# Kernel tuning notes

Hardware: AMD Instinct MI355X
Metric: run time of the kernel (lower is better)

The kernel has to match this reference:

```python
import jax, jax.numpy as jnp
import numpy as np

N = 100000
E = 1600000
G = 128


def _degrees(src, dst, n):
    ones = jnp.ones(src.shape[0], dtype=jnp.float32)
    deg_out = jax.ops.segment_sum(ones, src, num_segments=n)
    deg_in = jax.ops.segment_sum(ones, dst, num_segments=n)
    return jnp.maximum(deg_out, 1.0), jnp.maximum(deg_in, 1.0)


def gcn_conv(x, W, b, src, dst, norm_out, norm_in):
    # DGL GraphConv, norm='both': scale src by d_out^-1/2, sum over edges,
    # scale dst by d_in^-1/2, then linear. Weight applied first (out<=in) --
    # mathematically identical, cheaper gather.
    h = (x * norm_out[:, None]) @ W          # [N, out]
    m = h[src]                               # [E, out] gather
    agg = jax.ops.segment_sum(m, dst, num_segments=N)  # [N, out] scatter-add
    return agg * norm_in[:, None] + b


def setup_inputs() -> dict:
    key = jax.random.key(0)
    ks = jax.random.split(key, 8)
    x = jax.random.normal(ks[0], (N, 128), dtype=jnp.float32)
    W1 = jax.random.normal(ks[1], (128, 64), dtype=jnp.float32) * (1.0 / np.sqrt(128))
    b1 = jnp.zeros((64,), dtype=jnp.float32)
    W2 = jax.random.normal(ks[2], (64, 16), dtype=jnp.float32) * (1.0 / np.sqrt(64))
    b2 = jnp.zeros((16,), dtype=jnp.float32)
    src = jax.random.randint(ks[3], (E,), 0, N, dtype=jnp.int32)
    dst = jax.random.randint(ks[4], (E,), 0, N, dtype=jnp.int32)
    graph_ids = jnp.sort(jax.random.randint(ks[5], (N,), 0, G, dtype=jnp.int32))
    return {"x": x, "W1": W1, "b1": b1, "W2": W2, "b2": b2,
            "src": src, "dst": dst, "graph_ids": graph_ids}


def reference(x, W1, b1, W2, b2, src, dst, graph_ids):
    deg_out, deg_in = _degrees(src, dst, N)
    norm_out = jax.lax.rsqrt(deg_out)
    norm_in = jax.lax.rsqrt(deg_in)
    h = gcn_conv(x, W1, b1, src, dst, norm_out, norm_in)
    h = jax.nn.relu(h)
    # dropout(p=0.2) is identity in eval mode
    h = gcn_conv(h, W2, b2, src, dst, norm_out, norm_in)
    # dgl.mean_nodes: per-graph mean pooling
    sums = jax.ops.segment_sum(h, graph_ids, num_segments=G)      # [G, 16]
    counts = jax.ops.segment_sum(jnp.ones((N,), jnp.float32), graph_ids, num_segments=G)
    return sums / jnp.maximum(counts, 1.0)[:, None]
```

## Files before the change

### kernel.cpp

```cpp
#include <hip/hip_runtime.h>
#include <hip/hip_fp16.h>

#define N_NODES 100000
#define N_EDGES 1600000
#define N_GRAPHS 128
#define SB 391
#define CAP 4608
#define NBLK 512
#define NE4 (N_EDGES / 4)
#define CH4 782
#define LDX 136

typedef unsigned long long u64;
typedef unsigned int u32;
typedef unsigned char u8;
typedef _Float16 f16;
typedef f16 half8 __attribute__((ext_vector_type(8)));
typedef f16 half4v __attribute__((ext_vector_type(4)));
typedef f16 half2v __attribute__((ext_vector_type(2)));
typedef float floatx4 __attribute__((ext_vector_type(4)));

__global__ void k_init(int* __restrict__ cur_d, int* __restrict__ cur_s) {
  int t = blockIdx.x * blockDim.x + threadIdx.x;
  if (t < SB) { cur_d[t] = t * CAP; cur_s[t] = t * CAP; }
}

__global__ __launch_bounds__(256) void k_fuse(const int4* __restrict__ src4,
                                              const int4* __restrict__ dst4,
                                              int* __restrict__ cur_d,
                                              int* __restrict__ cur_s,
                                              u32* __restrict__ ed,
                                              u8* __restrict__ ssk8) {
  __shared__ int hd[SB], hs[SB], ld[SB], ls[SB];
  const int t = threadIdx.x, b = blockIdx.x;
  for (int j = t; j < SB; j += 256) { hd[j] = 0; hs[j] = 0; }
  __syncthreads();
  const int start = b * CH4, end = min(start + CH4, NE4);
  for (int i = start + t; i < end; i += 256) {
    int4 d = dst4[i]; int4 s = src4[i];
    atomicAdd(&hd[d.x >> 8], 1); atomicAdd(&hd[d.y >> 8], 1);
    atomicAdd(&hd[d.z >> 8], 1); atomicAdd(&hd[d.w >> 8], 1);
    atomicAdd(&hs[s.x >> 8], 1); atomicAdd(&hs[s.y >> 8], 1);
    atomicAdd(&hs[s.z >> 8], 1); atomicAdd(&hs[s.w >> 8], 1);
  }
  __syncthreads();
  for (int j = t; j < SB; j += 256) {
    ld[j] = atomicAdd(&cur_d[j], hd[j]);
    ls[j] = atomicAdd(&cur_s[j], hs[j]);
  }
  __syncthreads();
  for (int i = start + t; i < end; i += 256) {
    int4 d4 = dst4[i]; int4 s4 = src4[i];
    {
      int d = d4.x, s = s4.x;
      int pd = atomicAdd(&ld[d >> 8], 1);
      ed[pd] = ((u32)(d & 255) << 24) | (u32)s;
      int ps = atomicAdd(&ls[s >> 8], 1);
      ssk8[ps] = (u8)(s & 255);
    }
    {
      int d = d4.y, s = s4.y;
      int pd = atomicAdd(&ld[d >> 8], 1);
      ed[pd] = ((u32)(d & 255) << 24) | (u32)s;
      int ps = atomicAdd(&ls[s >> 8], 1);
      ssk8[ps] = (u8)(s & 255);
    }
    {
      int d = d4.z, s = s4.z;
      int pd = atomicAdd(&ld[d >> 8], 1);
      ed[pd] = ((u32)(d & 255) << 24) | (u32)s;
      int ps = atomicAdd(&ls[s >> 8], 1);
      ssk8[ps] = (u8)(s & 255);
    }
    {
      int d = d4.w, s = s4.w;
      int pd = atomicAdd(&ld[d >> 8], 1);
      ed[pd] = ((u32)(d & 255) << 24) | (u32)s;
      int ps = atomicAdd(&ls[s >> 8], 1);
      ssk8[ps] = (u8)(s & 255);
    }
  }
}

__global__ __launch_bounds__(256) void k_bucket_csr(const u32* __restrict__ ed,
                                                    const u8* __restrict__ ssk8,
                                                    const int* __restrict__ cur_d,
                                                    const int* __restrict__ cur_s,
                                                    int* __restrict__ row_ptr,
                                                    int* __restrict__ deg,
                                                    float* __restrict__ norm_in,
                                                    float* __restrict__ norm_out,
                                                    int* __restrict__ edge_src) {
  __shared__ int hist[256], scanbuf[256], cursor[256], hist2[256];
  const int b = blockIdx.x, t = threadIdx.x;
  const int base = b << 8;
  const int lo = b * CAP;
  const int hiD = cur_d[b];
  const int hiS = cur_s[b];
  hist[t] = 0; hist2[t] = 0;
  __syncthreads();
  for (int i = lo + t; i < hiS; i += 256) atomicAdd(&hist2[ssk8[i]], 1);
  for (int i = lo + t; i < hiD; i += 256) atomicAdd(&hist[ed[i] >> 24], 1);
  __syncthreads();
  int node = base + t;
  if (node < N_NODES)
    norm_out[node] = rsqrtf(fmaxf((float)hist2[t], 1.0f));
  int v = hist[t];
  scanbuf[t] = v;
  __syncthreads();
  for (int off = 1; off < 256; off <<= 1) {
    int a = (t >= off) ? scanbuf[t - off] : 0;
    __syncthreads(); scanbuf[t] += a; __syncthreads();
  }
  int excl = scanbuf[t] - v;
  if (node < N_NODES) {
    row_ptr[node] = lo + excl;
    deg[node] = v;
    norm_in[node] = rsqrtf(fmaxf((float)v, 1.0f));
  }
  cursor[t] = excl;
  __syncthreads();
  for (int i = lo + t; i < hiD; i += 256) {
    u32 e = ed[i];
    int p = atomicAdd(&cursor[e >> 24], 1);
    edge_src[lo + p] = (int)(e & 0x00FFFFFFu);
  }
}

__global__ __launch_bounds__(256) void k_gemm1(const float* __restrict__ x,
                                               const float* __restrict__ W1,
                                               const float* __restrict__ norm_out,
                                               __half* __restrict__ h1h) {
  __shared__ __align__(16) f16 Xs[64 * LDX];
  __shared__ __align__(16) f16 Ws[64 * LDX];
  const int t = threadIdx.x;
  const int row0 = blockIdx.x * 64;

  const float4* W4 = (const float4*)W1;
  for (int i = t; i < 2048; i += 256) {
    int k = i >> 4, n4 = (i & 15) * 4;
    float4 v = W4[i];
    Ws[(n4 + 0) * LDX + k] = (f16)v.x;
    Ws[(n4 + 1) * LDX + k] = (f16)v.y;
    Ws[(n4 + 2) * LDX + k] = (f16)v.z;
    Ws[(n4 + 3) * LDX + k] = (f16)v.w;
  }
  const float4* x4 = (const float4*)x;
  #pragma unroll
  for (int i = 0; i < 8; ++i) {
    int idx = t + 256 * i;
    int r = idx >> 5, c4 = idx & 31;
    int row = row0 + r;
    float4 v = make_float4(0.f, 0.f, 0.f, 0.f);
    if (row < N_NODES) {
      float s = norm_out[row];
      v = x4[(size_t)row * 32 + c4];
      v.x *= s; v.y *= s; v.z *= s; v.w *= s;
    }
    half4v h = { (f16)v.x, (f16)v.y, (f16)v.z, (f16)v.w };
    *(half4v*)&Xs[r * LDX + c4 * 4] = h;
  }
  __syncthreads();

  const int w = t >> 6, l = t & 63;
  const int m = l & 15, quad = l >> 4;
  floatx4 c0 = {0.f,0.f,0.f,0.f}, c1 = {0.f,0.f,0.f,0.f};
  floatx4 c2 = {0.f,0.f,0.f,0.f}, c3 = {0.f,0.f,0.f,0.f};
  const f16* xrow = &Xs[(w * 16 + m) * LDX + quad * 8];
  const f16* wrow = &Ws[m * LDX + quad * 8];
  #pragma unroll
  for (int kb = 0; kb < 4; ++kb) {
    half8 a  = *(const half8*)(xrow + kb * 32);
    half8 b0 = *(const half8*)(wrow + kb * 32);
    half8 b1 = *(const half8*)(wrow + 16 * LDX + kb * 32);
    half8 b2 = *(const half8*)(wrow + 32 * LDX + kb * 32);
    half8 b3 = *(const half8*)(wrow + 48 * LDX + kb * 32);
    c0 = __builtin_amdgcn_mfma_f32_16x16x32_f16(a, b0, c0, 0, 0, 0);
    c1 = __builtin_amdgcn_mfma_f32_16x16x32_f16(a, b1, c1, 0, 0, 0);
    c2 = __builtin_amdgcn_mfma_f32_16x16x32_f16(a, b2, c2, 0, 0, 0);
    c3 = __builtin_amdgcn_mfma_f32_16x16x32_f16(a, b3, c3, 0, 0, 0);
  }
  #pragma unroll
  for (int r = 0; r < 4; ++r) {
    int row = row0 + w * 16 + quad * 4 + r;
    if (row < N_NODES + 1) {
      __half* dst = h1h + (size_t)row * 64 + m;
      dst[0]  = __float2half(c0[r]);
      dst[16] = __float2half(c1[r]);
      dst[32] = __float2half(c2[r]);
      dst[48] = __float2half(c3[r]);
    }
  }
}

__global__ __launch_bounds__(256) void k_gather_l1(const int* __restrict__ row_ptr,
                                                   const int* __restrict__ deg,
                                                   const int* __restrict__ edge_src,
                                                   const __half* __restrict__ h1h,
                                                   const float* __restrict__ norm_in,
                                                   const float* __restrict__ norm_out,
                                                   const float* __restrict__ b1,
                                                   const float* __restrict__ W2,
                                                   __half* __restrict__ h2h) {
  __shared__ __align__(16) f16 Rs[16 * 72];
  __shared__ __align__(16) f16 Ws2[16 * 72];
  const int t = threadIdx.x;
  for (int i = t; i < 1024; i += 256) {
    int k = i >> 4, n = i & 15;
    Ws2[n * 72 + k] = (f16)W2[i];
  }
  if (blockIdx.x == 0 && t < 16) h2h[(size_t)N_NODES * 16 + t] = __float2half(0.f);

  const int w = t >> 6;
  const int l = t & 63;
  const int hf = l >> 5;
  const u32 c = (u32)(l & 31);

  const u32* __restrict__ h1u = (const u32*)h1h;
  const float2 bb = ((const float2*)b1)[c];
  const int base = blockIdx.x * 16;

  #pragma unroll 1
  for (int i4 = 0; i4 < 4; ++i4) {
    const int n = base + w * 4 + i4;
    const int lo = row_ptr[n], hi = lo + deg[n];

    float2 a0 = {0.f,0.f}, a1 = {0.f,0.f}, a2 = {0.f,0.f}, a3 = {0.f,0.f};
    float2 a4 = {0.f,0.f}, a5 = {0.f,0.f}, a6 = {0.f,0.f}, a7 = {0.f,0.f};
    for (int i = lo; i < hi; i += 16) {
      int idx = i + (l & 15);
      int sv = (idx < hi) ? edge_src[idx] : (int)N_NODES;
      int s0 = __shfl(sv,  0 + hf, 64);
      int s1 = __shfl(sv,  2 + hf, 64);
      int s2 = __shfl(sv,  4 + hf, 64);
      int s3 = __shfl(sv,  6 + hf, 64);
      int s4 = __shfl(sv,  8 + hf, 64);
      int s5 = __shfl(sv, 10 + hf, 64);
      int s6 = __shfl(sv, 12 + hf, 64);
      int s7 = __shfl(sv, 14 + hf, 64);
      u32 v0 = h1u[(u32)s0 * 32u + c];
      u32 v1 = h1u[(u32)s1 * 32u + c];
      u32 v2 = h1u[(u32)s2 * 32u + c];
      u32 v3 = h1u[(u32)s3 * 32u + c];
      u32 v4 = h1u[(u32)s4 * 32u + c];
      u32 v5 = h1u[(u32)s5 * 32u + c];
      u32 v6 = h1u[(u32)s6 * 32u + c];
      u32 v7 = h1u[(u32)s7 * 32u + c];
      float2 f;
      f = __half22float2(*(__half2*)&v0); a0.x += f.x; a0.y += f.y;
      f = __half22float2(*(__half2*)&v1); a1.x += f.x; a1.y += f.y;
      f = __half22float2(*(__half2*)&v2); a2.x += f.x; a2.y += f.y;
      f = __half22float2(*(__half2*)&v3); a3.x += f.x; a3.y += f.y;
      f = __half22float2(*(__half2*)&v4); a4.x += f.x; a4.y += f.y;
      f = __half22float2(*(__half2*)&v5); a5.x += f.x; a5.y += f.y;
      f = __half22float2(*(__half2*)&v6); a6.x += f.x; a6.y += f.y;
      f = __half22float2(*(__half2*)&v7); a7.x += f.x; a7.y += f.y;
    }
    float accx = ((a0.x + a1.x) + (a2.x + a3.x)) + ((a4.x + a5.x) + (a6.x + a7.x));
    float accy = ((a0.y + a1.y) + (a2.y + a3.y)) + ((a4.y + a5.y) + (a6.y + a7.y));
    accx += __shfl_xor(accx, 32, 64);
    accy += __shfl_xor(accy, 32, 64);

    const float ni = norm_in[n];
    float h1x = fmaxf(accx * ni + bb.x, 0.0f);
    float h1y = fmaxf(accy * ni + bb.y, 0.0f);
    if (l < 32) {
      half2v hv = { (f16)h1x, (f16)h1y };
      *(half2v*)&Rs[(w * 4 + i4) * 72 + 2 * (int)c] = hv;
    }
  }
  __syncthreads();

  if (w == 0) {
    const int m = l & 15, q = l >> 4;
    const f16* ra = &Rs[m * 72 + q * 8];
    const f16* rb = &Ws2[m * 72 + q * 8];
    half8 a0 = *(const half8*)ra;
    half8 a1 = *(const half8*)(ra + 32);
    half8 b0 = *(const half8*)rb;
    half8 b1v = *(const half8*)(rb + 32);
    floatx4 cc = {0.f,0.f,0.f,0.f};
    cc = __builtin_amdgcn_mfma_f32_16x16x32_f16(a0, b0, cc, 0, 0, 0);
    cc = __builtin_amdgcn_mfma_f32_16x16x32_f16(a1, b1v, cc, 0, 0, 0);
    #pragma unroll
    for (int r = 0; r < 4; ++r) {
      int row = base + q * 4 + r;
      h2h[(size_t)row * 16 + m] = __float2half(cc[r] * norm_out[row]);
    }
  }
}

__global__ __launch_bounds__(256) void k_gather_l2(const int* __restrict__ row_ptr,
                                                   const int* __restrict__ deg,
                                                   const int* __restrict__ edge_src,
                                                   const __half* __restrict__ h2h,
                                                   const float* __restrict__ norm_in,
                                                   float* __restrict__ agg2) {
  const int t = threadIdx.x;
  const int w = t >> 6;
  const int l = t & 63;
  const int n = blockIdx.x * 4 + w;
  const int f2 = l & 7;
  const int p = l >> 3;

  const u32* __restrict__ h2u = (const u32*)h2h;
  const int lo = row_ptr[n], hi = lo + deg[n];

  float ax = 0.f, ay = 0.f, bx = 0.f, by = 0.f;
  for (int base = lo; base < hi; base += 16) {
    int i1 = base + p, i2 = base + p + 8;
    int s0 = (i1 < hi) ? edge_src[i1] : (int)N_NODES;
    int s1 = (i2 < hi) ? edge_src[i2] : (int)N_NODES;
    u32 v0 = h2u[(u32)s0 * 8u + (u32)f2];
    u32 v1 = h2u[(u32)s1 * 8u + (u32)f2];
    float2 g0 = __half22float2(*(__half2*)&v0);
    float2 g1 = __half22float2(*(__half2*)&v1);
    ax += g0.x; ay += g0.y;
    bx += g1.x; by += g1.y;
  }
  float sx = ax + bx, sy = ay + by;
  sx += __shfl_xor(sx, 8, 64);  sy += __shfl_xor(sy, 8, 64);
  sx += __shfl_xor(sx, 16, 64); sy += __shfl_xor(sy, 16, 64);
  sx += __shfl_xor(sx, 32, 64); sy += __shfl_xor(sy, 32, 64);
  if (l < 8) {
    float ni = norm_in[n];
    ((float2*)agg2)[(size_t)n * 8 + f2] = make_float2(sx * ni, sy * ni);
  }
}

__global__ __launch_bounds__(256) void k_pool(const float* __restrict__ agg2,
                                              const float* __restrict__ b2,
                                              const int* __restrict__ gid,
                                              float* __restrict__ out) {
  const int g = blockIdx.x;
  __shared__ int s_lo, s_hi;
  if (threadIdx.x == 0) {
    int a = 0, b = N_NODES;
    while (a < b) { int m = (a + b) >> 1; if (gid[m] < g) a = m + 1; else b = m; }
    s_lo = a;
    b = N_NODES;
    while (a < b) { int m = (a + b) >> 1; if (gid[m] < g + 1) a = m + 1; else b = m; }
    s_hi = a;
  }
  __syncthreads();
  const int lo = s_lo, hi = s_hi, cnt = hi - lo;
  const int j = threadIdx.x & 15;
  const int r = threadIdx.x >> 4;
  float acc = 0.f;
  for (int n = lo + r; n < hi; n += 16)
    acc += agg2[(size_t)n * 16 + j];

  __shared__ float red[256];
  red[threadIdx.x] = acc;
  __syncthreads();
  #pragma unroll
  for (int s = 8; s > 0; s >>= 1) {
    if (r < s) red[threadIdx.x] += red[threadIdx.x + s * 16];
    __syncthreads();
  }
  if (r == 0)
    out[g * 16 + j] = (cnt > 0) ? (red[j] / (float)cnt + b2[j]) : 0.0f;
}

extern "C" void kernel_launch(void* const* d_in, const int* in_sizes, int n_in,
                              void* d_out, int out_size, void* d_ws, size_t ws_size,
                              hipStream_t stream) {
  const float* x   = (const float*)d_in[0];
  const float* W1  = (const float*)d_in[1];
  const float* b1  = (const float*)d_in[2];
  const float* W2  = (const float*)d_in[3];
  const float* b2  = (const float*)d_in[4];
  const int*   src = (const int*)d_in[5];
  const int*   dst = (const int*)d_in[6];
  const int*   gid = (const int*)d_in[7];
  float* out = (float*)d_out;

  int* wsi = (int*)d_ws;
  float* wsf = (float*)d_ws;

  float* norm_out = wsf + 0;
  float* norm_in  = wsf + 100000;
  int*   row_ptr  = wsi + 200000;
  int*   deg      = wsi + 300000;
  int*   cur_d    = wsi + 400000;
  int*   cur_s    = wsi + 400400;
  int*   edge_src = wsi + 400800;
  const size_t S  = 2202528;
  u8*    ssk8     = (u8*)(wsi + S);
  u32*   ed       = (u32*)(wsi + S + 450432);
  __half* h1h     = (__half*)(wsi + S);
  __half* h2h     = (__half*)(wsi + S + 3200032);
  float*  agg2    = (float*)(wsi + S);

  const int4* src4 = (const int4*)src;
  const int4* dst4 = (const int4*)dst;

  k_init      <<<2, 256, 0, stream>>>(cur_d, cur_s);
  k_fuse      <<<NBLK, 256, 0, stream>>>(src4, dst4, cur_d, cur_s, ed, ssk8);
  k_bucket_csr<<<SB, 256, 0, stream>>>(ed, ssk8, cur_d, cur_s, row_ptr, deg,
                                       norm_in, norm_out, edge_src);
  k_gemm1     <<<(N_NODES + 64) / 64, 256, 0, stream>>>(x, W1, norm_out, h1h);
  k_gather_l1 <<<N_NODES / 16, 256, 0, stream>>>(row_ptr, deg, edge_src, h1h,
                                                 norm_in, norm_out, b1, W2, h2h);
  k_gather_l2 <<<N_NODES / 4, 256, 0, stream>>>(row_ptr, deg, edge_src, h2h,
                                                norm_in, agg2);
  k_pool      <<<N_GRAPHS, 256, 0, stream>>>(agg2, b2, gid, out);
}
```

Before: 266.5 us.

## Aggregate layer-1 neighbor features with MFMA segment-sum over contiguous CSR edge ranges

Rewrites the layer-1 gather so that each wave handles 16 consecutive destination nodes as one contiguous edge range. Neighbor rows are loaded as 16-byte vectors and the segment sum is done with MFMA: an identity matrix transposes the gathered rows and a 0/1 mask matrix selects the edges belonging to each node. The next chunk's loads are prefetched while the current chunk is computed, and the per-wave LDS tile now feeds the W2 MFMA directly without a block-wide barrier. The transposed partial sums are rounded to fp16 before accumulation, which adds precision risk. MFMA work is also wasted on masked edges, because every node in the group scans the whole range of the group.

```diff
diff --git a/kernel.cpp b/kernel.cpp
--- a/kernel.cpp
+++ b/kernel.cpp
@@ -17,7 +17,6 @@
 typedef _Float16 f16;
 typedef f16 half8 __attribute__((ext_vector_type(8)));
 typedef f16 half4v __attribute__((ext_vector_type(4)));
-typedef f16 half2v __attribute__((ext_vector_type(2)));
 typedef float floatx4 __attribute__((ext_vector_type(4)));
 
 __global__ void k_init(int* __restrict__ cur_d, int* __restrict__ cur_s) {
@@ -202,91 +201,125 @@
                                                    const float* __restrict__ b1,
                                                    const float* __restrict__ W2,
                                                    __half* __restrict__ h2h) {
-  __shared__ __align__(16) f16 Rs[16 * 72];
   __shared__ __align__(16) f16 Ws2[16 * 72];
+  __shared__ __align__(16) f16 Rs[4][16 * 72];
   const int t = threadIdx.x;
   for (int i = t; i < 1024; i += 256) {
     int k = i >> 4, n = i & 15;
     Ws2[n * 72 + k] = (f16)W2[i];
   }
   if (blockIdx.x == 0 && t < 16) h2h[(size_t)N_NODES * 16 + t] = __float2half(0.f);
-
-  const int w = t >> 6;
-  const int l = t & 63;
-  const int hf = l >> 5;
-  const u32 c = (u32)(l & 31);
-
-  const u32* __restrict__ h1u = (const u32*)h1h;
-  const float2 bb = ((const float2*)b1)[c];
-  const int base = blockIdx.x * 16;
-
+  __syncthreads();
+
+  const int w = t >> 6, l = t & 63;
+  const int base = blockIdx.x * 64 + w * 16;
+  if (base >= N_NODES) return;
+
+  const int m = l & 15, q4 = l >> 4;
+  const int node_l = min(base + m, N_NODES - 1);
+  const int my_lo = row_ptr[node_l];
+  const u32 my_deg = (u32)deg[node_l];
+  const int lo_blk = __shfl(my_lo, 0, 64);
+  const int hi_blk = __shfl(my_lo + (int)my_deg, 15, 64);
+
+  const int s1e = 8 * (m >> 2) + (m & 3);
+  const int s2e = s1e + 4;
+
+  union U4 { u32 u[4]; half8 h; uint4 v; };
+
+  U4 ib0, ib1;
+  #pragma unroll
+  for (int wj = 0; wj < 4; ++wj) {
+    int k0 = q4 * 8 + 2 * wj, k1 = k0 + 1;
+    ib0.u[wj] = (k0 == m      ? 0x3C00u : 0u) | (k1 == m      ? 0x3C000000u : 0u);
+    ib1.u[wj] = (k0 == m + 16 ? 0x3C00u : 0u) | (k1 == m + 16 ? 0x3C000000u : 0u);
+  }
+
+  const uint4* __restrict__ h1u4 = (const uint4*)h1h;
+  floatx4 acc0 = {0.f,0.f,0.f,0.f}, acc1 = {0.f,0.f,0.f,0.f};
+  floatx4 acc2 = {0.f,0.f,0.f,0.f}, acc3 = {0.f,0.f,0.f,0.f};
+  const floatx4 zf = {0.f,0.f,0.f,0.f};
+
+  uint4 pa0, pa1, pb0, pb1;
+  #define LOADC(CB) do {                                                      \
+    int i1 = (CB) + s1e, i2 = (CB) + s2e;                                     \
+    int sv1 = (i1 < hi_blk) ? edge_src[i1] : (int)N_NODES;                    \
+    int sv2 = (i2 < hi_blk) ? edge_src[i2] : (int)N_NODES;                    \
+    size_t r1 = (size_t)(u32)sv1 * 8u, r2 = (size_t)(u32)sv2 * 8u;            \
+    pa0 = h1u4[r1 + (u32)q4];       pa1 = h1u4[r1 + 4u + (u32)q4];            \
+    pb0 = h1u4[r2 + (u32)q4];       pb1 = h1u4[r2 + 4u + (u32)q4];            \
+  } while (0)
+
+  if (lo_blk < hi_blk) LOADC(lo_blk);
   #pragma unroll 1
-  for (int i4 = 0; i4 < 4; ++i4) {
-    const int n = base + w * 4 + i4;
-    const int lo = row_ptr[n], hi = lo + deg[n];
-
-    float2 a0 = {0.f,0.f}, a1 = {0.f,0.f}, a2 = {0.f,0.f}, a3 = {0.f,0.f};
-    float2 a4 = {0.f,0.f}, a5 = {0.f,0.f}, a6 = {0.f,0.f}, a7 = {0.f,0.f};
-    for (int i = lo; i < hi; i += 16) {
-      int idx = i + (l & 15);
-      int sv = (idx < hi) ? edge_src[idx] : (int)N_NODES;
-      int s0 = __shfl(sv,  0 + hf, 64);
-      int s1 = __shfl(sv,  2 + hf, 64);
-      int s2 = __shfl(sv,  4 + hf, 64);
-      int s3 = __shfl(sv,  6 + hf, 64);
-      int s4 = __shfl(sv,  8 + hf, 64);
-      int s5 = __shfl(sv, 10 + hf, 64);
-      int s6 = __shfl(sv, 12 + hf, 64);
-      int s7 = __shfl(sv, 14 + hf, 64);
-      u32 v0 = h1u[(u32)s0 * 32u + c];
-      u32 v1 = h1u[(u32)s1 * 32u + c];
-      u32 v2 = h1u[(u32)s2 * 32u + c];
-      u32 v3 = h1u[(u32)s3 * 32u + c];
-      u32 v4 = h1u[(u32)s4 * 32u + c];
-      u32 v5 = h1u[(u32)s5 * 32u + c];
-      u32 v6 = h1u[(u32)s6 * 32u + c];
-      u32 v7 = h1u[(u32)s7 * 32u + c];
-      float2 f;
-      f = __half22float2(*(__half2*)&v0); a0.x += f.x; a0.y += f.y;
-      f = __half22float2(*(__half2*)&v1); a1.x += f.x; a1.y += f.y;
-      f = __half22float2(*(__half2*)&v2); a2.x += f.x; a2.y += f.y;
-      f = __half22float2(*(__half2*)&v3); a3.x += f.x; a3.y += f.y;
-      f = __half22float2(*(__half2*)&v4); a4.x += f.x; a4.y += f.y;
-      f = __half22float2(*(__half2*)&v5); a5.x += f.x; a5.y += f.y;
-      f = __half22float2(*(__half2*)&v6); a6.x += f.x; a6.y += f.y;
-      f = __half22float2(*(__half2*)&v7); a7.x += f.x; a7.y += f.y;
-    }
-    float accx = ((a0.x + a1.x) + (a2.x + a3.x)) + ((a4.x + a5.x) + (a6.x + a7.x));
-    float accy = ((a0.y + a1.y) + (a2.y + a3.y)) + ((a4.y + a5.y) + (a6.y + a7.y));
-    accx += __shfl_xor(accx, 32, 64);
-    accy += __shfl_xor(accy, 32, 64);
-
-    const float ni = norm_in[n];
-    float h1x = fmaxf(accx * ni + bb.x, 0.0f);
-    float h1y = fmaxf(accy * ni + bb.y, 0.0f);
-    if (l < 32) {
-      half2v hv = { (f16)h1x, (f16)h1y };
-      *(half2v*)&Rs[(w * 4 + i4) * 72 + 2 * (int)c] = hv;
-    }
-  }
-  __syncthreads();
-
-  if (w == 0) {
-    const int m = l & 15, q = l >> 4;
-    const f16* ra = &Rs[m * 72 + q * 8];
-    const f16* rb = &Ws2[m * 72 + q * 8];
-    half8 a0 = *(const half8*)ra;
-    half8 a1 = *(const half8*)(ra + 32);
-    half8 b0 = *(const half8*)rb;
-    half8 b1v = *(const half8*)(rb + 32);
-    floatx4 cc = {0.f,0.f,0.f,0.f};
-    cc = __builtin_amdgcn_mfma_f32_16x16x32_f16(a0, b0, cc, 0, 0, 0);
-    cc = __builtin_amdgcn_mfma_f32_16x16x32_f16(a1, b1v, cc, 0, 0, 0);
-    #pragma unroll
-    for (int r = 0; r < 4; ++r) {
-      int row = base + q * 4 + r;
+  for (int cb = lo_blk; cb < hi_blk; cb += 32) {
+    U4 ca0, ca1, cbb0, cbb1;
+    ca0.v = pa0; ca1.v = pa1; cbb0.v = pb0; cbb1.v = pb1;
+    if (cb + 32 < hi_blk) LOADC(cb + 32);
+
+    u32 e0 = (u32)(cb - my_lo) + (u32)(q4 * 8);
+    U4 s;
+    s.u[0] = ((e0+0u)<my_deg?0x3C00u:0u) | ((e0+1u)<my_deg?0x3C000000u:0u);
+    s.u[1] = ((e0+2u)<my_deg?0x3C00u:0u) | ((e0+3u)<my_deg?0x3C000000u:0u);
+    s.u[2] = ((e0+4u)<my_deg?0x3C00u:0u) | ((e0+5u)<my_deg?0x3C000000u:0u);
+    s.u[3] = ((e0+6u)<my_deg?0x3C00u:0u) | ((e0+7u)<my_deg?0x3C000000u:0u);
+
+    {
+      floatx4 o10 = __builtin_amdgcn_mfma_f32_16x16x32_f16(ca0.h,  ib0.h, zf, 0, 0, 0);
+      floatx4 o11 = __builtin_amdgcn_mfma_f32_16x16x32_f16(ca0.h,  ib1.h, zf, 0, 0, 0);
+      floatx4 o20 = __builtin_amdgcn_mfma_f32_16x16x32_f16(cbb0.h, ib0.h, zf, 0, 0, 0);
+      floatx4 o21 = __builtin_amdgcn_mfma_f32_16x16x32_f16(cbb0.h, ib1.h, zf, 0, 0, 0);
+      half8 bf0 = { (f16)o10[0], (f16)o10[1], (f16)o10[2], (f16)o10[3],
+                    (f16)o20[0], (f16)o20[1], (f16)o20[2], (f16)o20[3] };
+      half8 bf1 = { (f16)o11[0], (f16)o11[1], (f16)o11[2], (f16)o11[3],
+                    (f16)o21[0], (f16)o21[1], (f16)o21[2], (f16)o21[3] };
+      acc0 = __builtin_amdgcn_mfma_f32_16x16x32_f16(s.h, bf0, acc0, 0, 0, 0);
+      acc1 = __builtin_amdgcn_mfma_f32_16x16x32_f16(s.h, bf1, acc1, 0, 0, 0);
+    }
+    {
+      floatx4 o10 = __builtin_amdgcn_mfma_f32_16x16x32_f16(ca1.h,  ib0.h, zf, 0, 0, 0);
+      floatx4 o11 = __builtin_amdgcn_mfma_f32_16x16x32_f16(ca1.h,  ib1.h, zf, 0, 0, 0);
+      floatx4 o20 = __builtin_amdgcn_mfma_f32_16x16x32_f16(cbb1.h, ib0.h, zf, 0, 0, 0);
+      floatx4 o21 = __builtin_amdgcn_mfma_f32_16x16x32_f16(cbb1.h, ib1.h, zf, 0, 0, 0);
+      half8 bf0 = { (f16)o10[0], (f16)o10[1], (f16)o10[2], (f16)o10[3],
+                    (f16)o20[0], (f16)o20[1], (f16)o20[2], (f16)o20[3] };
+      half8 bf1 = { (f16)o11[0], (f16)o11[1], (f16)o11[2], (f16)o11[3],
+                    (f16)o21[0], (f16)o21[1], (f16)o21[2], (f16)o21[3] };
+      acc2 = __builtin_amdgcn_mfma_f32_16x16x32_f16(s.h, bf0, acc2, 0, 0, 0);
+      acc3 = __builtin_amdgcn_mfma_f32_16x16x32_f16(s.h, bf1, acc3, 0, 0, 0);
+    }
+  }
+  #undef LOADC
+
+  const float bg0 = b1[m], bg1 = b1[16 + m], bg2 = b1[32 + m], bg3 = b1[48 + m];
+  f16* Rw = &Rs[w][0];
+  #pragma unroll
+  for (int r = 0; r < 4; ++r) {
+    int row = base + q4 * 4 + r;
+    float ni = (row < N_NODES) ? norm_in[row] : 0.f;
+    f16* dst = &Rw[(q4 * 4 + r) * 72 + m];
+    dst[0]  = (f16)fmaxf(acc0[r] * ni + bg0, 0.f);
+    dst[16] = (f16)fmaxf(acc1[r] * ni + bg1, 0.f);
+    dst[32] = (f16)fmaxf(acc2[r] * ni + bg2, 0.f);
+    dst[48] = (f16)fmaxf(acc3[r] * ni + bg3, 0.f);
+  }
+  asm volatile("s_waitcnt lgkmcnt(0)" ::: "memory");
+  __builtin_amdgcn_sched_barrier(0);
+
+  const f16* ra = &Rw[m * 72 + q4 * 8];
+  const f16* rb = &Ws2[m * 72 + q4 * 8];
+  half8 a0 = *(const half8*)ra;
+  half8 a1 = *(const half8*)(ra + 32);
+  half8 wb0 = *(const half8*)rb;
+  half8 wb1 = *(const half8*)(rb + 32);
+  floatx4 cc = {0.f,0.f,0.f,0.f};
+  cc = __builtin_amdgcn_mfma_f32_16x16x32_f16(a0, wb0, cc, 0, 0, 0);
+  cc = __builtin_amdgcn_mfma_f32_16x16x32_f16(a1, wb1, cc, 0, 0, 0);
+  #pragma unroll
+  for (int r = 0; r < 4; ++r) {
+    int row = base + q4 * 4 + r;
+    if (row < N_NODES)
       h2h[(size_t)row * 16 + m] = __float2half(cc[r] * norm_out[row]);
-    }
   }
 }
 
@@ -400,8 +433,8 @@
   k_bucket_csr<<<SB, 256, 0, stream>>>(ed, ssk8, cur_d, cur_s, row_ptr, deg,
                                        norm_in, norm_out, edge_src);
   k_gemm1     <<<(N_NODES + 64) / 64, 256, 0, stream>>>(x, W1, norm_out, h1h);
-  k_gather_l1 <<<N_NODES / 16, 256, 0, stream>>>(row_ptr, deg, edge_src, h1h,
-                                                 norm_in, norm_out, b1, W2, h2h);
+  k_gather_l1 <<<(N_NODES + 63) / 64, 256, 0, stream>>>(row_ptr, deg, edge_src, h1h,
+                                                        norm_in, norm_out, b1, W2, h2h);
   k_gather_l2 <<<N_NODES / 4, 256, 0, stream>>>(row_ptr, deg, edge_src, h2h,
                                                 norm_in, agg2);
   k_pool      <<<N_GRAPHS, 256, 0, stream>>>(agg2, b2, gid, out);
```

New measurement: 267.4 us. No clear change (+0.3%).
